# Kernel tuning notes

Measured on AMD Instinct MI355X. Metric: run time of the kernel, lower is better.

## Reference

```python
import jax, jax.numpy as jnp
import numpy as np

B, T, D_IN, D_OUT, H = 4, 2048, 768, 768, 12
HD = D_OUT // H  # 64


def setup_inputs() -> dict:
    key = jax.random.key(0)
    ks = jax.random.split(key, 6)
    s_in = 1.0 / np.sqrt(D_IN)
    s_out = 1.0 / np.sqrt(D_OUT)
    return {
        "x": jax.random.normal(ks[0], (B, T, D_IN), dtype=jnp.float32),
        "Wq": jax.random.uniform(ks[1], (D_IN, D_OUT), jnp.float32, -s_in, s_in),
        "Wk": jax.random.uniform(ks[2], (D_IN, D_OUT), jnp.float32, -s_in, s_in),
        "Wv": jax.random.uniform(ks[3], (D_IN, D_OUT), jnp.float32, -s_in, s_in),
        "Wo": jax.random.uniform(ks[4], (D_OUT, D_OUT), jnp.float32, -s_out, s_out),
        "bo": jax.random.uniform(ks[5], (D_OUT,), jnp.float32, -s_out, s_out),
    }


def reference(x, Wq, Wk, Wv, Wo, bo):
    b, t, _ = x.shape
    # QKV projections (no bias, per qkv_bias=False), split into heads: [b,h,t,hd]
    q = (x @ Wq).reshape(b, t, H, HD).transpose(0, 2, 1, 3)
    k = (x @ Wk).reshape(b, t, H, HD).transpose(0, 2, 1, 3)
    v = (x @ Wv).reshape(b, t, H, HD).transpose(0, 2, 1, 3)
    # NOTE: original calls masked_fill (non-in-place) and discards the result,
    # so NO causal mask is actually applied. Faithfully reproduce that.
    scores = jnp.einsum("bhqd,bhkd->bhqk", q, k)  # [b,h,t,t]
    attn = jax.nn.softmax(scores / jnp.sqrt(jnp.float32(HD)), axis=-1)
    # dropout p=0.0 (eval) -> identity
    ctx = jnp.einsum("bhqk,bhkd->bhqd", attn, v)  # [b,h,t,hd]
    ctx = ctx.transpose(0, 2, 1, 3).reshape(b, t, D_OUT)
    return ctx @ Wo + bo
```

## Files before the change

kernel.cpp:

```cpp
#include <hip/hip_runtime.h>
#include <hip/hip_bf16.h>
#include <stdint.h>


#define HH   12
#define TT   2048
#define DIN  768
#define DOUT 768
#define HD   64
#define BB   4
#define MTOT (BB*TT)
#define NQKV (3*DOUT)
#define QSCALE 0.1803368801111832f

typedef float  float4v  __attribute__((ext_vector_type(4)));
typedef float  float16v __attribute__((ext_vector_type(16)));
typedef __bf16 bf16x8   __attribute__((ext_vector_type(8)));
typedef short  short8v  __attribute__((ext_vector_type(8)));

#define AS1 __attribute__((address_space(1)))
#define AS3 __attribute__((address_space(3)))

static __device__ __forceinline__ void gload_lds16(const void* g, void* l) {
    __builtin_amdgcn_global_load_lds((AS1 void*)g, (AS3 void*)l, 16, 0, 0);
}

static __device__ __forceinline__ short f2bf(float f) {
    __bf16 h = (__bf16)f;
    return __builtin_bit_cast(short, h);
}

__global__ __launch_bounds__(256) void cast_x_kernel(const float* __restrict__ x,
                                                     short* __restrict__ xb, int n4) {
    int i = blockIdx.x * 256 + threadIdx.x;
    if (i >= n4) return;
    float4 v = ((const float4*)x)[i];
    short4 o;
    o.x = f2bf(v.x); o.y = f2bf(v.y); o.z = f2bf(v.z); o.w = f2bf(v.w);
    ((short4*)xb)[i] = o;
}

__global__ __launch_bounds__(256) void prep_w_kernel(const float* __restrict__ Wq,
                                                     const float* __restrict__ Wk,
                                                     const float* __restrict__ Wv,
                                                     const float* __restrict__ Wo,
                                                     short* __restrict__ Wqkvt,
                                                     short* __restrict__ Wot) {
    __shared__ short tile[32 * 33];
    const int bx = blockIdx.x, by = blockIdx.y, bz = blockIdx.z;
    const float* W = (bz == 0) ? Wq : (bz == 1) ? Wk : (bz == 2) ? Wv : Wo;
    const int tx = threadIdx.x & 31, ty = threadIdx.x >> 5;
    for (int i = 0; i < 4; i++) {
        int k = by * 32 + ty + i * 8;
        tile[(ty + i * 8) * 33 + tx] = f2bf(W[(size_t)k * DOUT + bx * 32 + tx]);
    }
    __syncthreads();
    for (int i = 0; i < 4; i++) {
        int n = bx * 32 + ty + i * 8;
        int k = by * 32 + tx;
        short v = tile[tx * 33 + ty + i * 8];
        if (bz < 3) Wqkvt[(size_t)(bz * DOUT + n) * DIN + k] = v;
        else        Wot[(size_t)n * DOUT + k] = v;
    }
}

__global__ __launch_bounds__(256) void qkv_gemm_kernel(const short* __restrict__ Xb,
                                                       const short* __restrict__ Wt,
                                                       short* __restrict__ Qb,
                                                       short* __restrict__ Kb,
                                                       short* __restrict__ Vt) {
    __shared__ __align__(16) short lds[16384];
    short* ldsA = lds;
    short* ldsB = lds + 8192;
    const int t = threadIdx.x;
    const int w = t >> 6, lane = t & 63;
    const int quad = lane >> 4, l15 = lane & 15;
    const int m0 = blockIdx.x * 128, n0 = blockIdx.y * 128;
    const int wm = (w >> 1) * 64, wn = (w & 1) * 64;

    float4v acc[4][4];
    for (int i = 0; i < 4; i++)
        for (int j = 0; j < 4; j++)
            acc[i][j] = (float4v)0.0f;

    const int rA = t >> 3;
    const int cS = ((t & 7) ^ ((t >> 3) & 7)) * 8;
    const short* gA0 = Xb + (size_t)(m0 + rA) * DIN + cS;
    const short* gB0 = Wt + (size_t)(n0 + rA) * DIN + cS;

    for (int k0 = 0; k0 < DIN; k0 += 64) {
#pragma unroll
        for (int g = 0; g < 4; g++)
            gload_lds16(gA0 + (size_t)g * 32 * DIN + k0, &ldsA[(g * 256 + t) * 8]);
#pragma unroll
        for (int g = 0; g < 4; g++)
            gload_lds16(gB0 + (size_t)g * 32 * DIN + k0, &ldsB[(g * 256 + t) * 8]);
        __syncthreads();
#pragma unroll
        for (int kk = 0; kk < 2; kk++) {
            bf16x8 af[4], bfr[4];
            const int pos = ((kk * 4 + quad) ^ (l15 & 7)) * 8;
            for (int i = 0; i < 4; i++) af[i]  = *(const bf16x8*)&ldsA[(wm + i * 16 + l15) * 64 + pos];
            for (int j = 0; j < 4; j++) bfr[j] = *(const bf16x8*)&ldsB[(wn + j * 16 + l15) * 64 + pos];
            for (int i = 0; i < 4; i++)
                for (int j = 0; j < 4; j++)
                    acc[i][j] = __builtin_amdgcn_mfma_f32_16x16x32_bf16(af[i], bfr[j], acc[i][j], 0, 0, 0);
        }
        __syncthreads();
    }

    const int which = n0 / DOUT;
    if (which < 2) {
        short* ldsT = lds;
        const float sc = (which == 0) ? QSCALE : 1.0f;
        short* dst = (which == 0) ? Qb : Kb;
        const int n0sec = n0 - which * DOUT;
        for (int i = 0; i < 4; i++)
            for (int j = 0; j < 4; j++) {
                int col = wn + j * 16 + l15;
                int cx = col >> 3, co = col & 7;
                for (int r = 0; r < 4; r++) {
                    int row = wm + i * 16 + quad * 4 + r;
                    ldsT[row * 128 + ((cx ^ (row & 7)) * 8 + co)] = f2bf(acc[i][j][r] * sc);
                }
            }
        __syncthreads();
        for (int p = 0; p < 8; p++) {
            int row = p * 16 + (t >> 4);
            int cL = t & 15;
            short8v v = *(const short8v*)&ldsT[row * 128 + ((cL ^ (row & 7)) * 8)];
            int mg = m0 + row;
            int b2 = mg >> 11, tq = mg & 2047;
            int colg = n0sec + cL * 8;
            int hh = colg >> 6, d = colg & 63;
            *(short8v*)&dst[((size_t)((b2 * HH + hh) * TT + tq) << 6) + d] = v;
        }
    } else {
        short* ldsT = lds;
        const int n0r = n0 - 2 * DOUT;
        const int b = m0 >> 11, tq0 = m0 & 2047;
        for (int i = 0; i < 4; i++)
            for (int j = 0; j < 4; j++)
                for (int r = 0; r < 4; r++) {
                    int nl = wn + j * 16 + l15;
                    int ml = wm + i * 16 + quad * 4 + r;
                    int c = ml >> 3, o = ml & 7;
                    ldsT[nl * 128 + ((c ^ (nl & 7)) * 8 + o)] = f2bf(acc[i][j][r]);
                }
        __syncthreads();
        for (int p = 0; p < 8; p++) {
            int nrow = p * 16 + (t >> 4);
            int cc = t & 15;
            short8v v = *(const short8v*)&ldsT[nrow * 128 + ((cc ^ (nrow & 7)) * 8)];
            int colg = n0r + nrow;
            int hh = colg >> 6, d = colg & 63;
            *(short8v*)&Vt[(size_t)((b * HH + hh) * HD + d) * TT + tq0 + cc * 8] = v;
        }
    }
}

__global__ __launch_bounds__(256, 3) void attn_kernel(const short* __restrict__ Qb,
                                                      const short* __restrict__ Kb,
                                                      const short* __restrict__ Vt,
                                                      short* __restrict__ Ctx) {
    __shared__ __align__(16) short ldsK[2][64 * 64];
    __shared__ __align__(16) short ldsV[2][64 * 64];
    __shared__ float lsb[256];
    const int t = threadIdx.x;
    const int w = t >> 6, lane = t & 63;
    const int half = lane >> 5, m = lane & 31;
    const int qg = w & 1, kt = w >> 1;
    const int bh = blockIdx.x;
    const int b = bh / HH, h = bh - b * HH;
    const int q0 = blockIdx.y * 128 + qg * 64;

    const short* Qbase = Qb + (size_t)bh * TT * HD;
    const short* Kbase = Kb + (size_t)bh * TT * HD;
    const short* Vbase = Vt + (size_t)bh * HD * TT;

    bf16x8 qf[2][4];
#pragma unroll
    for (int qh = 0; qh < 2; qh++)
#pragma unroll
        for (int s = 0; s < 4; s++)
            qf[qh][s] = *(const bf16x8*)&Qbase[(q0 + qh * 32 + m) * HD + s * 16 + half * 8];

    int kOff[2], vOff[2];
    {
        int r5 = t >> 3;
        int pi = ((r5 >> 3) & 1) * 16 + ((r5 >> 2) & 1) * 8 + ((r5 >> 4) & 1) * 4 + (r5 & 3);
#pragma unroll
        for (int g = 0; g < 2; g++) {
            kOff[g] = (g * 32 + pi) * 64 + (((t & 7) ^ (r5 & 7)) * 8);
            int vrow = g * 32 + r5;
            vOff[g] = vrow * TT + (((t & 7) ^ (vrow & 7)) * 8);
        }
    }

    auto stage = [&](int buf, int u0) {
#pragma unroll
        for (int g = 0; g < 2; g++)
            gload_lds16(Kbase + (size_t)u0 * 64 + kOff[g], &ldsK[buf][(g * 256 + t) * 8]);
#pragma unroll
        for (int g = 0; g < 2; g++)
            gload_lds16(Vbase + (size_t)u0 + vOff[g], &ldsV[buf][(g * 256 + t) * 8]);
    };

    float16v accO[2][2];
#pragma unroll
    for (int qh = 0; qh < 2; qh++)
#pragma unroll
        for (int dt = 0; dt < 2; dt++)
            accO[qh][dt] = (float16v)0.0f;
    float lsum[2] = {0.0f, 0.0f};

    stage(0, 0);

    for (int it = 0; it < TT / 64; ++it) {
        __syncthreads();
        const int buf = it & 1;
        if (it + 1 < TT / 64) stage(buf ^ 1, (it + 1) * 64);
        const short* K_ = &ldsK[buf][0];
        const short* V_ = &ldsV[buf][0];

        float16v st0 = (float16v)0.0f;
        float16v st1 = (float16v)0.0f;
        __builtin_amdgcn_s_setprio(1);
#pragma unroll
        for (int s = 0; s < 4; s++) {
            bf16x8 ka = *(const bf16x8*)&K_[(kt * 32 + m) * 64 + (((s * 2 + half) ^ (m & 7)) * 8)];
            st0 = __builtin_amdgcn_mfma_f32_32x32x16_bf16(ka, qf[0][s], st0, 0, 0, 0);
            st1 = __builtin_amdgcn_mfma_f32_32x32x16_bf16(ka, qf[1][s], st1, 0, 0, 0);
        }
        __builtin_amdgcn_s_setprio(0);

        bf16x8 ap[2][2];
#pragma unroll
        for (int qh = 0; qh < 2; qh++) {
            float pe[16];
#pragma unroll
            for (int i = 0; i < 16; i++)
                pe[i] = __builtin_amdgcn_exp2f(qh ? st1[i] : st0[i]);
#pragma unroll
            for (int i = 0; i < 4; i++) {
                ap[qh][0][i]     = (__bf16)pe[i];
                ap[qh][0][4 + i] = (__bf16)pe[8 + i];
                ap[qh][1][i]     = (__bf16)pe[4 + i];
                ap[qh][1][4 + i] = (__bf16)pe[12 + i];
            }
            float ps[8];
#pragma unroll
            for (int i = 0; i < 8; i++) ps[i] = pe[i] + pe[i + 8];
#pragma unroll
            for (int i = 0; i < 4; i++) ps[i] += ps[i + 4];
            ps[0] += ps[2]; ps[1] += ps[3];
            lsum[qh] += ps[0] + ps[1];
        }

        __builtin_amdgcn_s_setprio(1);
#pragma unroll
        for (int ks = 0; ks < 2; ks++)
#pragma unroll
            for (int dt = 0; dt < 2; dt++) {
                int row = dt * 32 + m;
                bf16x8 bv = *(const bf16x8*)&V_[row * 64 + (((kt * 4 + ks * 2 + half) ^ (row & 7)) * 8)];
                accO[0][dt] = __builtin_amdgcn_mfma_f32_32x32x16_bf16(ap[0][ks], bv, accO[0][dt], 0, 0, 0);
                accO[1][dt] = __builtin_amdgcn_mfma_f32_32x32x16_bf16(ap[1][ks], bv, accO[1][dt], 0, 0, 0);
            }
        __builtin_amdgcn_s_setprio(0);
    }

    __syncthreads();
    float* dump = (qg == 0) ? (float*)&ldsK[0][0] : (float*)&ldsV[0][0];
    if (kt == 1) {
#pragma unroll
        for (int qh = 0; qh < 2; qh++) {
#pragma unroll
            for (int dt = 0; dt < 2; dt++)
#pragma unroll
                for (int r = 0; r < 16; r++)
                    dump[((qh * 2 + dt) * 16 + r) * 64 + lane] = accO[qh][dt][r];
            lsb[(qg * 2 + qh) * 64 + lane] = lsum[qh];
        }
    }
    __syncthreads();
    if (kt == 0) {
#pragma unroll
        for (int qh = 0; qh < 2; qh++) {
#pragma unroll
            for (int dt = 0; dt < 2; dt++)
#pragma unroll
                for (int r = 0; r < 16; r++)
                    accO[qh][dt][r] += dump[((qh * 2 + dt) * 16 + r) * 64 + lane];
            lsum[qh] += lsb[(qg * 2 + qh) * 64 + lane];
        }
#pragma unroll
        for (int qh = 0; qh < 2; qh++) {
            float v = lsum[qh] + __shfl_xor(lsum[qh], 32);
            float linv = 1.0f / v;
#pragma unroll
            for (int s = 0; s < 4; s++)
#pragma unroll
                for (int i = 0; i < 4; i++) {
                    int reg = s * 4 + i;
                    int qrow = i + s * 8 + half * 4;
                    float ln = __shfl(linv, qrow);
                    int qg2 = q0 + qh * 32 + qrow;
                    size_t base = (size_t)(b * TT + qg2) * DOUT + h * HD + m;
                    Ctx[base]      = f2bf(accO[qh][0][reg] * ln);
                    Ctx[base + 32] = f2bf(accO[qh][1][reg] * ln);
                }
        }
    }
}

__global__ __launch_bounds__(256) void out_gemm_kernel(const short* __restrict__ Cb,
                                                       const short* __restrict__ Wot,
                                                       const float* __restrict__ bo,
                                                       float* __restrict__ out) {
    __shared__ __align__(16) short ldsA[64 * 32];
    __shared__ __align__(16) short ldsB[128 * 32];
    const int t = threadIdx.x;
    const int w = t >> 6, lane = t & 63;
    const int quad = lane >> 4, l15 = lane & 15;
    const int m0 = blockIdx.x * 64, n0 = blockIdx.y * 128;
    const int wn = w * 32;

    float4v acc[4][2];
    for (int i = 0; i < 4; i++)
        for (int j = 0; j < 2; j++)
            acc[i][j] = (float4v)0.0f;

    const int rA = t >> 2;
    const int cSw = ((t & 3) ^ ((t >> 3) & 3)) * 8;
    const short* gA0 = Cb + (size_t)(m0 + rA) * DOUT + cSw;
    const short* gB0 = Wot + (size_t)(n0 + rA) * DOUT + cSw;
    const int pos = (quad ^ ((l15 >> 1) & 3)) * 8;

    for (int k0 = 0; k0 < DOUT; k0 += 32) {
        gload_lds16(gA0 + k0,             &ldsA[t * 8]);
        gload_lds16(gB0 + k0,             &ldsB[t * 8]);
        gload_lds16(gB0 + 64 * DOUT + k0, &ldsB[(t + 256) * 8]);
        __syncthreads();
        bf16x8 af[4], bfr[2];
        for (int i = 0; i < 4; i++) af[i]  = *(const bf16x8*)&ldsA[(i * 16 + l15) * 32 + pos];
        for (int j = 0; j < 2; j++) bfr[j] = *(const bf16x8*)&ldsB[(wn + j * 16 + l15) * 32 + pos];
        for (int i = 0; i < 4; i++)
            for (int j = 0; j < 2; j++)
                acc[i][j] = __builtin_amdgcn_mfma_f32_16x16x32_bf16(af[i], bfr[j], acc[i][j], 0, 0, 0);
        __syncthreads();
    }

    for (int i = 0; i < 4; i++) {
        int m = m0 + i * 16 + quad * 4;
        for (int j = 0; j < 2; j++) {
            int n = n0 + wn + j * 16 + l15;
            float bias = bo[n];
            for (int r = 0; r < 4; r++)
                out[(size_t)(m + r) * DOUT + n] = acc[i][j][r] + bias;
        }
    }
}

extern "C" void kernel_launch(void* const* d_in, const int* in_sizes, int n_in,
                              void* d_out, int out_size, void* d_ws, size_t ws_size,
                              hipStream_t stream) {
    const float* x  = (const float*)d_in[0];
    const float* Wq = (const float*)d_in[1];
    const float* Wk = (const float*)d_in[2];
    const float* Wv = (const float*)d_in[3];
    const float* Wo = (const float*)d_in[4];
    const float* bo = (const float*)d_in[5];
    float* out = (float*)d_out;

    char* ws = (char*)d_ws;
    short* Xb    = (short*)(ws + 0);
    short* Wqkvt = (short*)(ws + 12582912);
    short* Wot   = (short*)(ws + 16121856);
    short* Qb    = (short*)(ws + 17301504);
    short* Kb    = (short*)(ws + 29884416);
    short* Vt    = (short*)(ws + 42467328);
    short* Cb    = (short*)(ws + 55050240);

    cast_x_kernel<<<(MTOT * DIN / 4 + 255) / 256, 256, 0, stream>>>(x, Xb, MTOT * DIN / 4);
    prep_w_kernel<<<dim3(24, 24, 4), 256, 0, stream>>>(Wq, Wk, Wv, Wo, Wqkvt, Wot);
    qkv_gemm_kernel<<<dim3(MTOT / 128, NQKV / 128), 256, 0, stream>>>(Xb, Wqkvt, Qb, Kb, Vt);
    attn_kernel<<<dim3(BB * HH, TT / 128), 256, 0, stream>>>(Qb, Kb, Vt, Cb);
    out_gemm_kernel<<<dim3(MTOT / 64, DOUT / 128), 256, 0, stream>>>(Cb, Wot, bo, out);
}
```

Baseline: 221.4 us.

## Merge prep kernels, widen out-GEMM K tile, pin attention waves per EU

Folds the x cast into the weight-transpose prep kernel so one launch does both: a grid-strided z-slice of 576 blocks casts x while the other slices transpose the weights. Doubles the out-projection GEMM K step from 32 to 64, using an 8-way XOR swizzle and two MFMA sub-steps per tile, which halves the number of barrier pairs. Replaces the attention launch-bounds occupancy hint with amdgpu_waves_per_eu(3,3). The risks are that the cast now runs on fewer blocks, so it may be less parallel, and that the out GEMM uses more LDS per block.

Result: no change. 218.1 us (-1.5%).

```diff
diff --git a/kernel.cpp b/kernel.cpp
--- a/kernel.cpp
+++ b/kernel.cpp
@@ -30,24 +30,28 @@
     return __builtin_bit_cast(short, h);
 }
 
-__global__ __launch_bounds__(256) void cast_x_kernel(const float* __restrict__ x,
-                                                     short* __restrict__ xb, int n4) {
-    int i = blockIdx.x * 256 + threadIdx.x;
-    if (i >= n4) return;
-    float4 v = ((const float4*)x)[i];
-    short4 o;
-    o.x = f2bf(v.x); o.y = f2bf(v.y); o.z = f2bf(v.z); o.w = f2bf(v.w);
-    ((short4*)xb)[i] = o;
-}
-
-__global__ __launch_bounds__(256) void prep_w_kernel(const float* __restrict__ Wq,
-                                                     const float* __restrict__ Wk,
-                                                     const float* __restrict__ Wv,
-                                                     const float* __restrict__ Wo,
-                                                     short* __restrict__ Wqkvt,
-                                                     short* __restrict__ Wot) {
+__global__ __launch_bounds__(256) void prep_kernel(const float* __restrict__ x,
+                                                   const float* __restrict__ Wq,
+                                                   const float* __restrict__ Wk,
+                                                   const float* __restrict__ Wv,
+                                                   const float* __restrict__ Wo,
+                                                   short* __restrict__ Xb,
+                                                   short* __restrict__ Wqkvt,
+                                                   short* __restrict__ Wot) {
     __shared__ short tile[32 * 33];
-    const int bx = blockIdx.x, by = blockIdx.y, bz = blockIdx.z;
+    const int bz = blockIdx.z;
+    if (bz == 4) {
+        const int n4 = MTOT * DIN / 4;
+        int i = (blockIdx.y * 24 + blockIdx.x) * 256 + threadIdx.x;
+        for (; i < n4; i += 24 * 24 * 256) {
+            float4 v = ((const float4*)x)[i];
+            short4 o;
+            o.x = f2bf(v.x); o.y = f2bf(v.y); o.z = f2bf(v.z); o.w = f2bf(v.w);
+            ((short4*)Xb)[i] = o;
+        }
+        return;
+    }
+    const int bx = blockIdx.x, by = blockIdx.y;
     const float* W = (bz == 0) ? Wq : (bz == 1) ? Wk : (bz == 2) ? Wv : Wo;
     const int tx = threadIdx.x & 31, ty = threadIdx.x >> 5;
     for (int i = 0; i < 4; i++) {
@@ -159,10 +163,12 @@
     }
 }
 
-__global__ __launch_bounds__(256, 3) void attn_kernel(const short* __restrict__ Qb,
-                                                      const short* __restrict__ Kb,
-                                                      const short* __restrict__ Vt,
-                                                      short* __restrict__ Ctx) {
+__global__ __launch_bounds__(256)
+__attribute__((amdgpu_waves_per_eu(3, 3)))
+void attn_kernel(const short* __restrict__ Qb,
+                 const short* __restrict__ Kb,
+                 const short* __restrict__ Vt,
+                 short* __restrict__ Ctx) {
     __shared__ __align__(16) short ldsK[2][64 * 64];
     __shared__ __align__(16) short ldsV[2][64 * 64];
     __shared__ float lsb[256];
@@ -318,8 +324,8 @@
                                                        const short* __restrict__ Wot,
                                                        const float* __restrict__ bo,
                                                        float* __restrict__ out) {
-    __shared__ __align__(16) short ldsA[64 * 32];
-    __shared__ __align__(16) short ldsB[128 * 32];
+    __shared__ __align__(16) short ldsA[64 * 64];
+    __shared__ __align__(16) short ldsB[128 * 64];
     const int t = threadIdx.x;
     const int w = t >> 6, lane = t & 63;
     const int quad = lane >> 4, l15 = lane & 15;
@@ -331,23 +337,29 @@
         for (int j = 0; j < 2; j++)
             acc[i][j] = (float4v)0.0f;
 
-    const int rA = t >> 2;
-    const int cSw = ((t & 3) ^ ((t >> 3) & 3)) * 8;
-    const short* gA0 = Cb + (size_t)(m0 + rA) * DOUT + cSw;
-    const short* gB0 = Wot + (size_t)(n0 + rA) * DOUT + cSw;
-    const int pos = (quad ^ ((l15 >> 1) & 3)) * 8;
-
-    for (int k0 = 0; k0 < DOUT; k0 += 32) {
-        gload_lds16(gA0 + k0,             &ldsA[t * 8]);
-        gload_lds16(gB0 + k0,             &ldsB[t * 8]);
-        gload_lds16(gB0 + 64 * DOUT + k0, &ldsB[(t + 256) * 8]);
-        __syncthreads();
-        bf16x8 af[4], bfr[2];
-        for (int i = 0; i < 4; i++) af[i]  = *(const bf16x8*)&ldsA[(i * 16 + l15) * 32 + pos];
-        for (int j = 0; j < 2; j++) bfr[j] = *(const bf16x8*)&ldsB[(wn + j * 16 + l15) * 32 + pos];
-        for (int i = 0; i < 4; i++)
-            for (int j = 0; j < 2; j++)
-                acc[i][j] = __builtin_amdgcn_mfma_f32_16x16x32_bf16(af[i], bfr[j], acc[i][j], 0, 0, 0);
+    const int rA = t >> 3;
+    const int cS = ((t & 7) ^ ((t >> 3) & 7)) * 8;
+    const short* gA0 = Cb + (size_t)(m0 + rA) * DOUT + cS;
+    const short* gB0 = Wot + (size_t)(n0 + rA) * DOUT + cS;
+
+    for (int k0 = 0; k0 < DOUT; k0 += 64) {
+#pragma unroll
+        for (int g = 0; g < 2; g++)
+            gload_lds16(gA0 + (size_t)g * 32 * DOUT + k0, &ldsA[(g * 256 + t) * 8]);
+#pragma unroll
+        for (int g = 0; g < 4; g++)
+            gload_lds16(gB0 + (size_t)g * 32 * DOUT + k0, &ldsB[(g * 256 + t) * 8]);
+        __syncthreads();
+#pragma unroll
+        for (int kk = 0; kk < 2; kk++) {
+            bf16x8 af[4], bfr[2];
+            const int pos = ((kk * 4 + quad) ^ (l15 & 7)) * 8;
+            for (int i = 0; i < 4; i++) af[i]  = *(const bf16x8*)&ldsA[(i * 16 + l15) * 64 + pos];
+            for (int j = 0; j < 2; j++) bfr[j] = *(const bf16x8*)&ldsB[(wn + j * 16 + l15) * 64 + pos];
+            for (int i = 0; i < 4; i++)
+                for (int j = 0; j < 2; j++)
+                    acc[i][j] = __builtin_amdgcn_mfma_f32_16x16x32_bf16(af[i], bfr[j], acc[i][j], 0, 0, 0);
+        }
         __syncthreads();
     }
 
@@ -382,8 +394,7 @@
     short* Vt    = (short*)(ws + 42467328);
     short* Cb    = (short*)(ws + 55050240);
 
-    cast_x_kernel<<<(MTOT * DIN / 4 + 255) / 256, 256, 0, stream>>>(x, Xb, MTOT * DIN / 4);
-    prep_w_kernel<<<dim3(24, 24, 4), 256, 0, stream>>>(Wq, Wk, Wv, Wo, Wqkvt, Wot);
+    prep_kernel<<<dim3(24, 24, 5), 256, 0, stream>>>(x, Wq, Wk, Wv, Wo, Xb, Wqkvt, Wot);
     qkv_gemm_kernel<<<dim3(MTOT / 128, NQKV / 128), 256, 0, stream>>>(Xb, Wqkvt, Qb, Kb, Vt);
     attn_kernel<<<dim3(BB * HH, TT / 128), 256, 0, stream>>>(Qb, Kb, Vt, Cb);
     out_gemm_kernel<<<dim3(MTOT / 64, DOUT / 128), 256, 0, stream>>>(Cb, Wot, bo, out);
```
